# Optimization experiments

Hardware: AMD Instinct MI355X
Metric: run time of the kernel (lower is better)

Reference implementation:

```python
import jax, jax.numpy as jnp
import numpy as np

N, D, K = 8192, 2048, 10000
EPS = 1e-12
COMMITMENT_COST = 0.25


def _l2_normalize(v, axis):
    # matches torch F.normalize(p=2): v / max(||v||, eps)
    n = jnp.linalg.norm(v, axis=axis, keepdims=True)
    return v / jnp.maximum(n, EPS)


def setup_inputs() -> dict:
    key = jax.random.key(0)
    kx, kw = jax.random.split(key)
    x = jax.random.normal(kx, (N, D), dtype=jnp.float32)
    # nn.Embedding weight initialized uniform(0, 3) per the module
    weight = jax.random.uniform(kw, (K, D), dtype=jnp.float32, minval=0.0, maxval=3.0)
    return {"x": x, "weight": weight}


def reference(x, weight):
    # --- get_code_indices ---
    xn = _l2_normalize(x, axis=1)          # [N, D]
    wn = _l2_normalize(weight, axis=1)     # [K, D]
    # ||xn||^2 + ||wn||^2 - 2 xn . wn  -> [N, K]
    distances = (
        jnp.sum(xn * xn, axis=1, keepdims=True)
        + jnp.sum(wn * wn, axis=1)
        - 2.0 * jnp.matmul(xn, wn.T)
    )
    encoding_indices = jnp.argmin(distances, axis=1)  # [N]
    # --- quantize (gathers the UN-normalized codebook, as in the module) ---
    quantized = weight[encoding_indices]              # [N, D]
    # --- training losses ---
    q_latent_loss = jnp.mean((quantized - jax.lax.stop_gradient(x)) ** 2)
    e_latent_loss = jnp.mean((x - jax.lax.stop_gradient(quantized)) ** 2)
    loss = q_latent_loss + COMMITMENT_COST * e_latent_loss
    # straight-through estimator
    quantized = x + jax.lax.stop_gradient(quantized - x)
    return quantized, loss, encoding_indices
```

## Files before the change

kernel.cpp:

```cpp
#include <hip/hip_runtime.h>
#include <math.h>

typedef unsigned short ushort_t;
typedef short short8 __attribute__((ext_vector_type(8)));
typedef short short4v __attribute__((ext_vector_type(4)));
typedef float f32x4  __attribute__((ext_vector_type(4)));

#define N_ROWS 8192
#define D_DIM  2048
#define K_CODES 10000
#define EPSF   1e-12f

#define BMT 128
#define BKT 64
#define KT_N 32
#define MT 64
#define NT 80
#define NGROUP 320

#define BAND_ADD  2e-5f
#define FBIG 1e30f

__device__ __forceinline__ unsigned short f2bf(float f) {
  unsigned u = __float_as_uint(f);
  unsigned r = (u + 0x7fffu + ((u >> 16) & 1u)) >> 16;
  return (unsigned short)r;
}
__device__ __forceinline__ float bf2f(unsigned short h) {
  return __uint_as_float(((unsigned)h) << 16);
}

__device__ __forceinline__ void stage16(const ushort_t* g, ushort_t* l) {
  __builtin_amdgcn_global_load_lds(
      (const __attribute__((address_space(1))) unsigned int*)g,
      (__attribute__((address_space(3))) unsigned int*)l, 16, 0, 0);
}

__global__ __launch_bounds__(256) void norm_hi_kernel(
    const float* __restrict__ src, ushort_t* __restrict__ hi,
    float* __restrict__ sq_out, float* __restrict__ inv_out,
    float* __restrict__ hn_out, float* __restrict__ ln_out, int nrows)
{
  const int wv   = threadIdx.x >> 6;
  const int lane = threadIdx.x & 63;
  const int row  = blockIdx.x * 4 + wv;
  if (row >= nrows) return;

  const float4* rp4 = (const float4*)(src + (size_t)row * D_DIM);
  float4 v[8];
  float s = 0.0f;
  #pragma unroll
  for (int j = 0; j < 8; ++j) {
    v[j] = rp4[lane + 64 * j];
    s += v[j].x*v[j].x + v[j].y*v[j].y + v[j].z*v[j].z + v[j].w*v[j].w;
  }
  #pragma unroll
  for (int off = 32; off > 0; off >>= 1) s += __shfl_xor(s, off, 64);
  const float inv = 1.0f / fmaxf(sqrtf(s), EPSF);

  float t = 0.0f, th = 0.0f, tl = 0.0f;
  #pragma unroll
  for (int j = 0; j < 8; ++j) {
    float e[4] = {v[j].x, v[j].y, v[j].z, v[j].w};
    unsigned short hb[4];
    #pragma unroll
    for (int i = 0; i < 4; ++i) {
      float xn = e[i] * inv;
      t += xn * xn;
      unsigned short h = f2bf(xn);
      hb[i] = h;
      float hf = bf2f(h);
      th += hf * hf;
      float l = xn - hf;
      tl += l * l;
    }
    *(short4v*)(hi + (size_t)row * D_DIM + (lane + 64 * j) * 4) = *(short4v*)hb;
  }
  #pragma unroll
  for (int off = 32; off > 0; off >>= 1) {
    t  += __shfl_xor(t,  off, 64);
    th += __shfl_xor(th, off, 64);
    tl += __shfl_xor(tl, off, 64);
  }
  if (lane == 0) {
    sq_out[row]  = t;
    hn_out[row]  = sqrtf(th);
    ln_out[row]  = sqrtf(tl);
    inv_out[row] = inv;
  }
}

__global__ __launch_bounds__(256) void wmax_kernel(
    const float* __restrict__ whn, const float* __restrict__ wln,
    float* __restrict__ wmax_out)
{
  int tid = threadIdx.x;
  float mh = 0.0f, ml = 0.0f;
  for (int k = tid; k < K_CODES; k += 256) {
    mh = fmaxf(mh, whn[k]);
    ml = fmaxf(ml, wln[k]);
  }
  __shared__ float sh[256], sl[256];
  sh[tid] = mh; sl[tid] = ml;
  __syncthreads();
  #pragma unroll
  for (int o = 128; o > 0; o >>= 1) {
    if (tid < o) {
      sh[tid] = fmaxf(sh[tid], sh[tid + o]);
      sl[tid] = fmaxf(sl[tid], sl[tid + o]);
    }
    __syncthreads();
  }
  if (tid == 0) { wmax_out[0] = sh[0]; wmax_out[1] = sl[0]; }
}

#define LEXLT(da, ia, db, ib) ((da) < (db) || ((da) == (db) && (ia) < (ib)))

#define STAGE_A(KKO) { \
  _Pragma("unroll") for (int j = 0; j < 4; ++j) \
    stage16(Ah + (size_t)(row0 + w4*32 + j*8 + sub) * D_DIM + (KKO) + lsl, \
            lA + w4*2048 + j*512); }

#define STAGE_B(KKO) { \
  _Pragma("unroll") for (int j = 0; j < 4; ++j) { \
    int rr = col0 + w4*32 + j*8 + sub; rr = rr < K_CODES ? rr : K_CODES - 1; \
    stage16(Bh + (size_t)rr * D_DIM + (KKO) + lsl, \
            lB + w4*2048 + j*512); } }

#define COMPUTE_HALF(AP, BP) { \
  _Pragma("unroll") for (int m = 0; m < 4; ++m) \
    af[m] = *(const short8*)((AP) + m*1024); \
  _Pragma("unroll") for (int n = 0; n < 4; ++n) \
    bf[n] = *(const short8*)((BP) + n*1024); \
  _Pragma("unroll") for (int m = 0; m < 4; ++m) \
  _Pragma("unroll") for (int n = 0; n < 4; ++n) \
    acc[m][n] = __builtin_amdgcn_mfma_f32_16x16x32_bf16( \
        af[m], bf[n], acc[m][n], 0, 0, 0); }

__global__ __launch_bounds__(256, 4) void dist_top2_kernel(
    const ushort_t* __restrict__ Ah, const ushort_t* __restrict__ Bh,
    const float* __restrict__ wsq,
    float* __restrict__ p1d, int* __restrict__ p1i, float* __restrict__ p2d)
{
  __shared__ ushort_t lA[8192];
  __shared__ ushort_t lB[8192];

  const int tid  = threadIdx.x;
  const int lane = tid & 63;
  const int w4   = tid >> 6;
  const int wm   = w4 >> 1;
  const int wn   = w4 & 1;
  const int t16  = lane & 15;
  const int h4   = lane >> 4;

  const int mtile = blockIdx.x & 63;
  const int ntile = blockIdx.x >> 6;
  const int row0 = mtile * BMT;
  const int col0 = ntile * BMT;

  const int sub = lane >> 3;
  const int lsl = ((lane & 7) ^ sub) * 8;

  const ushort_t* aP0 = &lA[(wm*64 + t16)*64 + ((h4       ^ (t16 & 7)) * 8)];
  const ushort_t* aP1 = &lA[(wm*64 + t16)*64 + (((4 + h4) ^ (t16 & 7)) * 8)];
  const ushort_t* bP0 = &lB[(wn*64 + t16)*64 + ((h4       ^ (t16 & 7)) * 8)];
  const ushort_t* bP1 = &lB[(wn*64 + t16)*64 + (((4 + h4) ^ (t16 & 7)) * 8)];

  f32x4 acc[4][4];
  #pragma unroll
  for (int m = 0; m < 4; ++m)
    #pragma unroll
    for (int n = 0; n < 4; ++n) acc[m][n] = (f32x4){0.f, 0.f, 0.f, 0.f};

  short8 af[4], bf[4];

  for (int kt = 0; kt < KT_N; ++kt) {
    const int kk = kt * BKT;
    STAGE_A(kk);
    STAGE_B(kk);
    __syncthreads();
    COMPUTE_HALF(aP0, bP0);
    COMPUTE_HALF(aP1, bP1);
    __syncthreads();
  }

  float wsqr[4]; int colr[4];
  #pragma unroll
  for (int n = 0; n < 4; ++n) {
    int col = col0 + wn * 64 + n * 16 + t16;
    colr[n] = col;
    wsqr[n] = (col < K_CODES) ? wsq[col] : FBIG * 10.0f;
  }
  #pragma unroll
  for (int m = 0; m < 4; ++m) {
    int rloc = wm * 64 + m * 16 + h4 * 4;
    #pragma unroll
    for (int j = 0; j < 4; ++j) {
      #pragma unroll
      for (int half = 0; half < 2; ++half) {
        int na = half * 2, nb = na + 1;
        float da = wsqr[na] - 2.0f * acc[m][na][j]; int ia = colr[na];
        float db = wsqr[nb] - 2.0f * acc[m][nb][j]; int ib = colr[nb];
        float d1, d2; int i1;
        if (LEXLT(db, ib, da, ia)) { d1 = db; i1 = ib; d2 = da; }
        else                       { d1 = da; i1 = ia; d2 = db; }
        #pragma unroll
        for (int off = 1; off < 16; off <<= 1) {
          float od1 = __shfl_xor(d1, off, 64);
          int   oi1 = __shfl_xor(i1, off, 64);
          float od2 = __shfl_xor(d2, off, 64);
          if (LEXLT(od1, oi1, d1, i1)) { d2 = fminf(d1, od2); d1 = od1; i1 = oi1; }
          else                         { d2 = fminf(od1, d2); }
        }
        if (t16 == 0) {
          int grow = row0 + rloc + j;
          int gid = ntile * 4 + wn * 2 + half;
          size_t o = (size_t)grow * NGROUP + gid;
          p1d[o] = d1; p1i[o] = i1; p2d[o] = d2;
        }
      }
    }
  }
}

__global__ __launch_bounds__(256) void refine_gather_kernel(
    const float* __restrict__ x, const float* __restrict__ w,
    const float* __restrict__ xsq, const float* __restrict__ xinv,
    const float* __restrict__ xhn, const float* __restrict__ xln,
    const float* __restrict__ wsq, const float* __restrict__ winv,
    const float* __restrict__ whn, const float* __restrict__ wln,
    const float* __restrict__ wmax,
    const float* __restrict__ p1d, const int* __restrict__ p1i,
    const float* __restrict__ p2d,
    float* __restrict__ out, float* __restrict__ lpart,
    float* __restrict__ idxf_out)
{
  const int wv   = threadIdx.x >> 6;
  const int lane = threadIdx.x & 63;
  const int row  = blockIdx.x * 4 + wv;

  const float xs = xsq[row], xh = xhn[row], xl = xln[row];
  const float whm = wmax[0], wlm = wmax[1];
  const float eps_max = 2.0f * (xl * whm + xh * wlm + xl * wlm) + BAND_ADD;

  float gd1[5], gd2[5], geps[5];
  int   gi1[5];
  float tmin = FBIG;
  float bmind = FBIG; int bmink = 0x7fffffff;
  #pragma unroll
  for (int s = 0; s < 5; ++s) {
    size_t o = (size_t)row * NGROUP + lane + 64 * s;
    float d1 = p1d[o]; int i1 = p1i[o]; float d2 = p2d[o];
    int is = i1 < K_CODES ? i1 : K_CODES - 1;
    float e1 = 2.0f * (xl * whn[is] + xh * wln[is] + xl * wln[is]) + BAND_ADD;
    gd1[s] = d1; gi1[s] = i1; gd2[s] = d2; geps[s] = e1;
    tmin = fminf(tmin, d1 + e1);
    if (d1 < bmind || (d1 == bmind && i1 < bmink)) { bmind = d1; bmink = i1; }
  }
  #pragma unroll
  for (int off = 1; off < 64; off <<= 1) tmin = fminf(tmin, __shfl_xor(tmin, off, 64));
  const float T = tmin;

  #pragma unroll
  for (int off = 1; off < 64; off <<= 1) {
    float od = __shfl_xor(bmind, off, 64);
    int   ok = __shfl_xor(bmink, off, 64);
    if (od < bmind || (od == bmind && ok < bmink)) { bmind = od; bmink = ok; }
  }
  const int kfirst = bmink;

  unsigned long long ms[5], mc[5];
  int ncand = 0, nscan = 0;
  #pragma unroll
  for (int s = 0; s < 5; ++s) {
    bool scan = (gd2[s] - eps_max <= T);
    bool cand = !scan && (gd1[s] - geps[s] <= T);
    ms[s] = __ballot(scan); mc[s] = __ballot(cand);
    nscan += __popcll(ms[s]); ncand += __popcll(mc[s]);
  }

  int bi = kfirst;
  if (!(nscan == 0 && ncand == 1)) {
    const float4* xr4 = (const float4*)(x + (size_t)row * D_DIM);
    const float xiv = xinv[row];
    float4 xv[8];
    #pragma unroll
    for (int j = 0; j < 8; ++j) {
      float4 v = xr4[lane + 64 * j];
      v.x *= xiv; v.y *= xiv; v.z *= xiv; v.w *= xiv;
      xv[j] = v;
    }

    float bd = INFINITY; bi = 0x7fffffff;
    auto refine = [&](int k) {
      const float4* wr4 = (const float4*)(w + (size_t)k * D_DIM);
      const float wiv = winv[k];
      float a = 0.0f;
      #pragma unroll
      for (int j = 0; j < 8; ++j) {
        float4 wvv = wr4[lane + 64 * j];
        a += xv[j].x * (wvv.x * wiv) + xv[j].y * (wvv.y * wiv)
           + xv[j].z * (wvv.z * wiv) + xv[j].w * (wvv.w * wiv);
      }
      #pragma unroll
      for (int off = 32; off > 0; off >>= 1) a += __shfl_xor(a, off, 64);
      float df = (xs + wsq[k]) - 2.0f * a;
      if (df < bd || (df == bd && k < bi)) { bd = df; bi = k; }
    };

    if (kfirst < K_CODES) refine(kfirst);

    #pragma unroll
    for (int s = 0; s < 5; ++s) {
      unsigned long long m = mc[s];
      while (m) {
        int lsrc = __ffsll(m) - 1; m &= m - 1;
        int k = __shfl(gi1[s], lsrc, 64);
        if (k == kfirst || k >= K_CODES) continue;
        float a1d = __shfl(gd1[s],  lsrc, 64);
        float a1e = __shfl(geps[s], lsrc, 64);
        if (a1d - a1e <= bd + BAND_ADD) refine(k);
      }
      m = ms[s];
      while (m) {
        int lsrc = __ffsll(m) - 1; m &= m - 1;
        float a2d = __shfl(gd2[s], lsrc, 64);
        if (a2d - eps_max > bd + BAND_ADD) continue;
        int k0 = (lsrc + 64 * s) * 32;
        for (int kk = 0; kk < 32; ++kk) {
          int k = k0 + kk;
          if (k < K_CODES) refine(k);
        }
      }
    }
  }

  {
    const float4* wr4 = (const float4*)(w + (size_t)bi * D_DIM);
    const float4* xr4 = (const float4*)(x + (size_t)row * D_DIM);
    float4* og = (float4*)(out + (size_t)row * D_DIM);
    float s = 0.0f;
    #pragma unroll
    for (int j = 0; j < 8; ++j) {
      float4 wvv = wr4[lane + 64 * j];
      float4 xvv = xr4[lane + 64 * j];
      og[lane + 64 * j] = wvv;
      float d0 = wvv.x - xvv.x, d1 = wvv.y - xvv.y;
      float d2 = wvv.z - xvv.z, d3 = wvv.w - xvv.w;
      s += d0 * d0 + d1 * d1 + d2 * d2 + d3 * d3;
    }
    #pragma unroll
    for (int off = 32; off > 0; off >>= 1) s += __shfl_xor(s, off, 64);
    if (lane == 0) { lpart[row] = s; idxf_out[row] = (float)bi; }
  }
}

__global__ __launch_bounds__(256) void loss_kernel(const float* __restrict__ lpart,
                                                   float* __restrict__ loss_out)
{
  int tid = threadIdx.x;
  double s = 0.0;
  for (int t = tid; t < N_ROWS; t += 256) s += (double)lpart[t];
  __shared__ double sd[256];
  sd[tid] = s;
  __syncthreads();
  #pragma unroll
  for (int o = 128; o > 0; o >>= 1) {
    if (tid < o) sd[tid] += sd[tid + o];
    __syncthreads();
  }
  if (tid == 0)
    loss_out[0] = (float)(1.25 * sd[0] / (double)((size_t)N_ROWS * (size_t)D_DIM));
}

extern "C" void kernel_launch(void* const* d_in, const int* in_sizes, int n_in,
                              void* d_out, int out_size, void* d_ws, size_t ws_size,
                              hipStream_t stream) {
  const float* x = (const float*)d_in[0];
  const float* w = (const float*)d_in[1];
  float* out = (float*)d_out;
  char*  ws  = (char*)d_ws;

  size_t off = 0;
  auto alloc = [&](size_t bytes) {
    size_t o = off;
    off = (off + bytes + 255) & ~(size_t)255;
    return o;
  };
  const size_t szA1 = (size_t)N_ROWS * D_DIM * 2;
  const size_t szB1 = (size_t)K_CODES * D_DIM * 2;
  const size_t szP  = (size_t)NGROUP * N_ROWS * 4;

  ushort_t* Bh = (ushort_t*)(ws + alloc(szB1));
  float* wsq  = (float*)(ws + alloc((size_t)K_CODES * 4));
  float* winv = (float*)(ws + alloc((size_t)K_CODES * 4));
  float* whn  = (float*)(ws + alloc((size_t)K_CODES * 4));
  float* wln  = (float*)(ws + alloc((size_t)K_CODES * 4));
  float* wmax = (float*)(ws + alloc(2 * 4));
  float* xsq  = (float*)(ws + alloc((size_t)N_ROWS * 4));
  float* xinv = (float*)(ws + alloc((size_t)N_ROWS * 4));
  float* xhn  = (float*)(ws + alloc((size_t)N_ROWS * 4));
  float* xln  = (float*)(ws + alloc((size_t)N_ROWS * 4));
  float* p1d  = (float*)(ws + alloc(szP));
  int*   p1i  = (int*)  (ws + alloc(szP));
  float* p2d  = (float*)(ws + alloc(szP));
  float* lpart = (float*)(ws + alloc((size_t)N_ROWS * 4));

  ushort_t* Ahp;
  if (ws_size >= off + szA1) {
    Ahp = (ushort_t*)(ws + alloc(szA1));
  } else {
    Ahp = (ushort_t*)out;
  }

  float* loss_out = out + (size_t)N_ROWS * D_DIM;
  float* idxf_out = loss_out + 1;

  norm_hi_kernel<<<N_ROWS / 4, 256, 0, stream>>>(
      x, Ahp, xsq, xinv, xhn, xln, N_ROWS);
  norm_hi_kernel<<<K_CODES / 4, 256, 0, stream>>>(
      w, Bh, wsq, winv, whn, wln, K_CODES);
  wmax_kernel<<<1, 256, 0, stream>>>(whn, wln, wmax);
  dist_top2_kernel<<<MT * NT, 256, 0, stream>>>(
      Ahp, Bh, wsq, p1d, p1i, p2d);
  refine_gather_kernel<<<N_ROWS / 4, 256, 0, stream>>>(
      x, w, xsq, xinv, xhn, xln, wsq, winv, whn, wln, wmax,
      p1d, p1i, p2d, out, lpart, idxf_out);
  loss_kernel<<<1, 256, 0, stream>>>(lpart, loss_out);
}
```

Before: 733.6 us.

## Merge norm kernels and remap GEMM tiles to XCDs for L2 reuse

Measured after the change: 728.1 us, median of 2. Within noise of the previous version (-0.8%).

```diff
diff --git a/kernel.cpp b/kernel.cpp
--- a/kernel.cpp
+++ b/kernel.cpp
@@ -36,15 +36,22 @@
       (__attribute__((address_space(3))) unsigned int*)l, 16, 0, 0);
 }
 
-__global__ __launch_bounds__(256) void norm_hi_kernel(
-    const float* __restrict__ src, ushort_t* __restrict__ hi,
-    float* __restrict__ sq_out, float* __restrict__ inv_out,
-    float* __restrict__ hn_out, float* __restrict__ ln_out, int nrows)
+__global__ __launch_bounds__(256) void norm_all_kernel(
+    const float* __restrict__ x, const float* __restrict__ w,
+    ushort_t* __restrict__ xhi, ushort_t* __restrict__ whi,
+    float* __restrict__ xsq, float* __restrict__ xinv,
+    float* __restrict__ xhn, float* __restrict__ xln,
+    float* __restrict__ wsq, float* __restrict__ winv,
+    float* __restrict__ whn, float* __restrict__ wln)
 {
   const int wv   = threadIdx.x >> 6;
   const int lane = threadIdx.x & 63;
-  const int row  = blockIdx.x * 4 + wv;
-  if (row >= nrows) return;
+  const int r    = blockIdx.x * 4 + wv;
+  const bool isx = r < N_ROWS;
+  const int row  = isx ? r : r - N_ROWS;
+  if (!isx && row >= K_CODES) return;
+  const float* src = isx ? x : w;
+  ushort_t* hi = isx ? xhi : whi;
 
   const float4* rp4 = (const float4*)(src + (size_t)row * D_DIM);
   float4 v[8];
@@ -83,10 +90,11 @@
     tl += __shfl_xor(tl, off, 64);
   }
   if (lane == 0) {
-    sq_out[row]  = t;
-    hn_out[row]  = sqrtf(th);
-    ln_out[row]  = sqrtf(tl);
-    inv_out[row] = inv;
+    if (isx) {
+      xsq[row] = t; xhn[row] = sqrtf(th); xln[row] = sqrtf(tl); xinv[row] = inv;
+    } else {
+      wsq[row] = t; whn[row] = sqrtf(th); wln[row] = sqrtf(tl); winv[row] = inv;
+    }
   }
 }
 
@@ -153,8 +161,12 @@
   const int t16  = lane & 15;
   const int h4   = lane >> 4;
 
-  const int mtile = blockIdx.x & 63;
-  const int ntile = blockIdx.x >> 6;
+  const int xcd = blockIdx.x & 7;
+  const int l   = blockIdx.x >> 3;
+  const int lm  = l & 15;
+  const int ln  = l >> 4;
+  const int mtile = (xcd & 3) * 16 + lm;
+  const int ntile = (xcd >> 2) * 40 + ln;
   const int row0 = mtile * BMT;
   const int col0 = ntile * BMT;
 
@@ -416,10 +428,8 @@
   float* loss_out = out + (size_t)N_ROWS * D_DIM;
   float* idxf_out = loss_out + 1;
 
-  norm_hi_kernel<<<N_ROWS / 4, 256, 0, stream>>>(
-      x, Ahp, xsq, xinv, xhn, xln, N_ROWS);
-  norm_hi_kernel<<<K_CODES / 4, 256, 0, stream>>>(
-      w, Bh, wsq, winv, whn, wln, K_CODES);
+  norm_all_kernel<<<(N_ROWS + K_CODES + 3) / 4, 256, 0, stream>>>(
+      x, w, Ahp, Bh, xsq, xinv, xhn, xln, wsq, winv, whn, wln);
   wmax_kernel<<<1, 256, 0, stream>>>(whn, wln, wmax);
   dist_top2_kernel<<<MT * NT, 256, 0, stream>>>(
       Ahp, Bh, wsq, p1d, p1i, p2d);
```
